# Kernel tuning notes

Hardware: AMD Instinct MI355X
Metric: run time of the kernel (lower is better)

Reference implementation:

```python
import jax, jax.numpy as jnp
import numpy as np
from jax import lax

D_MODEL = 96; D_STATE = 16; D_INNER = 192; DT_RANK = 6; K = 4
BSZ = 2; HH = 64; WW = 64


def setup_inputs() -> dict:
    key = jax.random.key(0)
    ks = jax.random.split(key, 16)
    f = lambda k, shape, s=0.02: (jax.random.normal(k, shape) * s).astype(jnp.float32)
    P = DT_RANK + 2 * D_STATE
    return {
        "x": jax.random.normal(ks[0], (BSZ, HH, WW, D_MODEL), jnp.float32),
        "W_in": f(ks[1], (2 * D_INNER, D_MODEL)),
        "b_in": jnp.zeros((2 * D_INNER,), jnp.float32),
        "conv_w": f(ks[2], (D_INNER, 1, 3, 3)),
        "conv_b": jnp.zeros((D_INNER,), jnp.float32),
        "W_xp": f(ks[3], (K * P, K * D_INNER)),
        "b_xp": jnp.zeros((K * P,), jnp.float32),
        "W_dt": f(ks[4], (K * D_INNER, K * DT_RANK)),
        "b_dt": f(ks[5], (K * D_INNER,), 0.1),
        "A_log": jax.random.normal(ks[6], (K * D_INNER, D_STATE), jnp.float32),
        "D_skip": jnp.ones((K * D_INNER,), jnp.float32),
        "dt_bias": jax.random.normal(ks[7], (K * D_INNER,), jnp.float32),
        "W_out": f(ks[8], (D_MODEL, D_INNER)),
        "b_out": jnp.zeros((D_MODEL,), jnp.float32),
        "gamma": jnp.ones((D_INNER,), jnp.float32),
        "beta": jnp.zeros((D_INNER,), jnp.float32),
    }


def cross_scan(x):
    # x: (B, D, H, W) -> (B, 4, D, L); dirs: row-major, col-major, and their reverses
    B, D, H, W = x.shape
    L = H * W
    x0 = x.reshape(B, D, L)
    x1 = jnp.swapaxes(x, 2, 3).reshape(B, D, L)
    return jnp.stack([x0, x1, x0[..., ::-1], x1[..., ::-1]], axis=1)


def cross_merge(ys):
    # ys: (B, 4, D, H, W) -> (B, D, L); inverse of cross_scan, summed
    B, Kk, D, H, W = ys.shape
    L = H * W
    yf = ys.reshape(B, Kk, D, L)
    y02 = yf[:, 0] + yf[:, 2, :, ::-1]
    y13 = yf[:, 1] + yf[:, 3, :, ::-1]
    y13 = jnp.swapaxes(y13.reshape(B, D, W, H), 2, 3).reshape(B, D, L)
    return y02 + y13


def selective_scan(u, dt, A, Bm, Cm, D_skip, dt_bias):
    # u, dt: (B,K,Dv,L); A: (K,Dv,N); Bm, Cm: (B,K,N,L); D_skip, dt_bias: (K,Dv)
    # NOTE: torch code repeats Bm/Cm across Dv; we broadcast instead (same math).
    dt = jax.nn.softplus(dt + dt_bias[None, :, :, None])
    dt_l = jnp.moveaxis(dt, -1, 0)   # (L,B,K,Dv)
    u_l = jnp.moveaxis(u, -1, 0)     # (L,B,K,Dv)
    B_l = jnp.moveaxis(Bm, -1, 0)    # (L,B,K,N)
    C_l = jnp.moveaxis(Cm, -1, 0)    # (L,B,K,N)

    def step(h, inp):
        dt_t, u_t, b_t, c_t = inp
        dA = jnp.exp(dt_t[..., None] * A[None])                 # (B,K,Dv,N)
        dBu = (dt_t * u_t)[..., None] * b_t[:, :, None, :]      # (B,K,Dv,N)
        h = dA * h + dBu
        y = jnp.einsum('bkdn,bkn->bkd', h, c_t)
        return h, y

    h0 = jnp.zeros(u.shape[:3] + (A.shape[-1],), u.dtype)
    _, ys = lax.scan(step, h0, (dt_l, u_l, B_l, C_l))
    ys = jnp.moveaxis(ys, 0, -1)  # (B,K,Dv,L)
    return ys + u * D_skip[None, :, :, None]


def reference(x, W_in, b_in, conv_w, conv_b, W_xp, b_xp, W_dt, b_dt,
              A_log, D_skip, dt_bias, W_out, b_out, gamma, beta):
    B, H, W, _ = x.shape
    L = H * W
    xz = x @ W_in.T + b_in
    xx, z = jnp.split(xz, 2, axis=-1)
    z = jax.nn.silu(z)
    xc = jnp.transpose(xx, (0, 3, 1, 2))  # (B, D, H, W)
    xc = lax.conv_general_dilated(xc, conv_w, (1, 1), 'SAME',
                                  feature_group_count=D_INNER,
                                  dimension_numbers=('NCHW', 'OIHW', 'NCHW'))
    xc = jax.nn.silu(xc + conv_b[None, :, None, None])

    xs = cross_scan(xc)                      # (B, K, D, L)
    xs_flat = xs.reshape(B, K * D_INNER, L)

    x_dbl = jnp.einsum('bcl,pc->bpl', xs_flat, W_xp) + b_xp[None, :, None]
    x_dbl = x_dbl.reshape(B, K, DT_RANK + 2 * D_STATE, L)
    dts, Bm, Cm = jnp.split(x_dbl, [DT_RANK, DT_RANK + D_STATE], axis=2)
    dts = dts.reshape(B, K * DT_RANK, L)
    dts = jnp.einsum('brl,dr->bdl', dts, W_dt) + b_dt[None, :, None]

    A = -jnp.exp(A_log).reshape(K, D_INNER, D_STATE)
    u = xs_flat.reshape(B, K, D_INNER, L)
    dt = dts.reshape(B, K, D_INNER, L)
    ys = selective_scan(u, dt, A, Bm, Cm,
                        D_skip.reshape(K, D_INNER), dt_bias.reshape(K, D_INNER))

    y = cross_merge(ys.reshape(B, K, D_INNER, H, W))  # (B, D, L)
    y = jnp.transpose(y.reshape(B, D_INNER, H, W), (0, 2, 3, 1))

    mu = jnp.mean(y, axis=-1, keepdims=True)
    var = jnp.mean(jnp.square(y - mu), axis=-1, keepdims=True)
    y = (y - mu) * lax.rsqrt(var + 1e-5) * gamma + beta
    y = y * z
    return y @ W_out.T + b_out
```

## Files before the change

kernel.cpp:

```cpp
#include <hip/hip_runtime.h>
#include <cstdint>
#include <cstddef>


#define CHUNK 16
#define NCK   256

#if __has_builtin(__builtin_amdgcn_exp2f)
#define EXP2(x) __builtin_amdgcn_exp2f(x)
#else
#define EXP2(x) exp2f(x)
#endif
#define LOG2E 1.44269504088896340736f
#define LN2   0.69314718055994530942f

typedef __attribute__((ext_vector_type(8))) short short8;
typedef __attribute__((ext_vector_type(8))) unsigned short ushort8;
typedef __attribute__((ext_vector_type(4))) float f32x4;

__device__ __forceinline__ float siluf(float x){ return x * (1.f/(1.f+__expf(-x))); }
__device__ __forceinline__ float softplus_fast(float v){
  float e  = EXP2(v*LOG2E);
  float sp = LN2*__log2f(1.f + e);
  return (v > 20.f) ? v : sp;
}
__device__ __forceinline__ unsigned short f2b(float f){
  uint32_t u = __float_as_uint(f);
  uint32_t r = (u + 0x7fffu + ((u>>16)&1u)) >> 16;
  return (unsigned short)r;
}

template<int KD, int STRA, int STRB>
__device__ __forceinline__ void micro_mm_T(const float (&As)[64][STRA], const float (&BsT)[KD][STRB],
                                           int tx, int ty, float (&acc)[4][4])
{
#pragma unroll 2
  for (int k4 = 0; k4 < KD/4; k4++){
    float a[4][4];
#pragma unroll
    for (int i = 0; i < 4; i++){
      float4 t = *(const float4*)&As[ty*4+i][k4*4];
      a[i][0]=t.x; a[i][1]=t.y; a[i][2]=t.z; a[i][3]=t.w;
    }
#pragma unroll
    for (int e = 0; e < 4; e++){
      float4 b = *(const float4*)&BsT[k4*4+e][tx*4];
#pragma unroll
      for (int i = 0; i < 4; i++){
        acc[i][0] = fmaf(a[i][e], b.x, acc[i][0]);
        acc[i][1] = fmaf(a[i][e], b.y, acc[i][1]);
        acc[i][2] = fmaf(a[i][e], b.z, acc[i][2]);
        acc[i][3] = fmaf(a[i][e], b.w, acc[i][3]);
      }
    }
  }
}

__global__ __launch_bounds__(256) void k_cast_w(
    const float* __restrict__ Wxp, unsigned short* __restrict__ Wf)
{
  int tid = blockIdx.x*256 + threadIdx.x;
  if (tid >= 18432) return;
  int lane = tid & 63; int rest = tid >> 6;
  int pt = rest % 6; rest /= 6;
  int k32 = rest & 3; rest >>= 2;
  int kc = rest % 6; int ph = rest / 6;
  int n = lane & 15, q = lane >> 4;
  int p = ph*96 + pt*16 + n;
  int kbase = kc*128 + k32*32 + q*8;
  unsigned short v[8];
#pragma unroll
  for (int j = 0; j < 8; j++)
    v[j] = (p < 152) ? f2b(Wxp[(size_t)p*768 + kbase + j]) : (unsigned short)0;
  *(ushort8*)(Wf + (size_t)tid*8) = *(ushort8*)v;
}

__global__ __launch_bounds__(256) void k_gemm_in(
    const float* __restrict__ x, const float* __restrict__ W,
    const float* __restrict__ bias, float* __restrict__ xx, float* __restrict__ zs)
{
  __shared__ float As[64][100];
  __shared__ float BsT[96][68];
  const int m0 = blockIdx.x*64, n0 = blockIdx.y*64;
  const int tid = threadIdx.x;
#pragma unroll
  for (int i = 0; i < 6; i++){
    int idx = tid + i*256;
    { int r = idx/24, c4 = idx%24;
      *(float4*)&As[r][c4*4] = *(const float4*)(x + (size_t)(m0+r)*96 + c4*4); }
    { int r = idx & 63, c4 = idx >> 6;
      float4 wv = *(const float4*)(W + (size_t)(n0+r)*96 + c4*4);
      BsT[c4*4+0][r]=wv.x; BsT[c4*4+1][r]=wv.y; BsT[c4*4+2][r]=wv.z; BsT[c4*4+3][r]=wv.w; }
  }
  __syncthreads();
  const int tx = tid & 15, ty = tid >> 4;
  float acc[4][4] = {};
  micro_mm_T<96,100,68>(As, BsT, tx, ty, acc);
#pragma unroll
  for (int i = 0; i < 4; i++){
    int m = m0 + ty*4 + i;
#pragma unroll
    for (int j = 0; j < 4; j++){
      int n = n0 + tx*4 + j;
      float v = acc[i][j] + bias[n];
      if (n < 192) xx[(size_t)m*192 + n] = v;
      else         zs[(size_t)m*192 + (n-192)] = siluf(v);
    }
  }
}

__global__ __launch_bounds__(256) void k_conv(
    const float* __restrict__ xx, const float* __restrict__ cw, const float* __restrict__ cb,
    float* __restrict__ xc,
    unsigned short* __restrict__ xcb, unsigned short* __restrict__ xcTb)
{
  int gid = blockIdx.x*256 + threadIdx.x;
  int c = gid % 192;
  int l = (gid/192) & 4095;
  int b = gid / (192*4096);
  int h = l >> 6, w = l & 63;
  float s = 0.f;
#pragma unroll
  for (int kh = 0; kh < 3; kh++){
    int h2 = h + kh - 1;
    if ((unsigned)h2 >= 64u) continue;
#pragma unroll
    for (int kw = 0; kw < 3; kw++){
      int w2 = w + kw - 1;
      if ((unsigned)w2 >= 64u) continue;
      s += xx[((size_t)b*4096 + h2*64 + w2)*192 + c] * cw[c*9 + kh*3 + kw];
    }
  }
  s = siluf(s + cb[c]);
  unsigned short sb = f2b(s);
  size_t i0 = ((size_t)b*4096 + l)*192 + c;
  xc[i0] = s; xcb[i0] = sb;
  int tl = (l & 63)*64 + (l >> 6);
  xcTb[((size_t)b*4096 + tl)*192 + c] = sb;
}

__global__ __launch_bounds__(256) void k_gemm_xdbl(
    const unsigned short* __restrict__ xcb, const unsigned short* __restrict__ xcTb,
    const unsigned short* __restrict__ Wf, const float* __restrict__ bxp,
    float* __restrict__ xdbl, float* __restrict__ dts_c)
{
  __shared__ unsigned short Bsh[4*6*64*8];
  const int tid = threadIdx.x;
  const int lane = tid & 63, w = tid >> 6;
  const int wl = w & 1, wp = w >> 1;
  const int l0 = blockIdx.x*64, ph = blockIdx.y, b = blockIdx.z;
  const int n = lane & 15, q = lane >> 4;
  f32x4 acc[2][3] = {};
  const unsigned short* slab0 = Wf + (size_t)ph*6*12288;
  for (int kc = 0; kc < 6; kc++){
    __syncthreads();
    const ushort8* srcp = (const ushort8*)(slab0 + (size_t)kc*12288);
#pragma unroll
    for (int t = 0; t < 6; t++) ((ushort8*)Bsh)[tid + t*256] = srcp[tid + t*256];
    __syncthreads();
#pragma unroll
    for (int k32 = 0; k32 < 4; k32++){
      int kk = kc*128 + k32*32;
      int dir = kk/192; int ch = kk%192 + q*8;
      const unsigned short* sp = (dir & 1) ? xcTb : xcb;
      bool rev = (dir >= 2);
      short8 a[2];
#pragma unroll
      for (int mt = 0; mt < 2; mt++){
        int ls = l0 + wl*32 + mt*16 + n;
        int row = rev ? 4095 - ls : ls;
        a[mt] = *(const short8*)(sp + ((size_t)b*4096 + row)*192 + ch);
      }
#pragma unroll
      for (int j = 0; j < 3; j++){
        short8 bfr = *(const short8*)&Bsh[((size_t)(k32*6 + wp*3 + j)*64 + lane)*8];
#pragma unroll
        for (int mt = 0; mt < 2; mt++)
          acc[mt][j] = __builtin_amdgcn_mfma_f32_16x16x32_bf16(a[mt], bfr, acc[mt][j], 0, 0, 0);
      }
    }
  }
#pragma unroll
  for (int mt = 0; mt < 2; mt++)
#pragma unroll
    for (int j = 0; j < 3; j++){
      int p = ph*96 + (wp*3+j)*16 + n;
      if (p < 152){
        int k = p/38, pp = p%38;
        int off = (pp < 6) ? pp : pp + 2;
        float bias = bxp[p];
#pragma unroll
        for (int reg = 0; reg < 4; reg++){
          int l = l0 + wl*32 + mt*16 + q*4 + reg;
          float val = acc[mt][j][reg] + bias;
          xdbl[(((size_t)b*4 + k)*4096 + l)*48 + off] = val;
          if (pp < 6) dts_c[((size_t)b*4096 + l)*24 + k*6 + pp] = val;
        }
      }
    }
}

__global__ __launch_bounds__(256) void k_scanA(
    const float* __restrict__ xc, const float* __restrict__ xdbl,
    const float* __restrict__ dts_c,
    const float* __restrict__ A_log, const float* __restrict__ Wdt,
    const float* __restrict__ bdt, const float* __restrict__ dtbias,
    float* __restrict__ dte, float* __restrict__ Pb, float* __restrict__ Sb)
{
  const int lane = threadIdx.x & 63;
  const int wid  = __builtin_amdgcn_readfirstlane(blockIdx.x*4 + (threadIdx.x >> 6));
  const int ck = wid & (NCK-1); const int g = wid / NCK;
  const int dblk = g % 3; const int bk = g / 3;
  const int k = bk & 3; const int b = bk >> 2;
  const int d = dblk*64 + lane; const int ch = k*192 + d;
  float An[16];
  {
    const float4* ap = (const float4*)(A_log + (size_t)ch*16);
#pragma unroll
    for (int i = 0; i < 4; i++){
      float4 t = ap[i];
      An[4*i+0] = -LOG2E*__expf(t.x); An[4*i+1] = -LOG2E*__expf(t.y);
      An[4*i+2] = -LOG2E*__expf(t.z); An[4*i+3] = -LOG2E*__expf(t.w);
    }
  }
  float Wr[24];
#pragma unroll
  for (int r = 0; r < 24; r++) Wr[r] = Wdt[(size_t)ch*24 + r];
  const float bsum = bdt[ch] + dtbias[ch];
  const int l0 = ck*CHUNK;
  const bool rev = (k >= 2);
  const int tr = k & 1;
  const int T0 = tr ? ((l0 & 63)*64 + (l0 >> 6)) : l0;
  const int rs = tr ? 64 : 1;
  const int row0 = rev ? 4095 - T0 : T0;
  const int rstep = (rev ? -rs : rs)*192;
  const float* up  = xc + ((size_t)b*4096 + row0)*192 + d;
  const float* qc  = dts_c + ((size_t)b*4096 + l0)*24;
  const float* xbc = xdbl + (((size_t)b*4 + k)*4096 + l0)*48;
  float* dtw = dte + (((size_t)b*4 + k)*4096 + l0)*192 + d;
  float h[16];
#pragma unroll
  for (int n = 0; n < 16; n++) h[n] = 0.f;
  float sdt = 0.f;
#pragma unroll 4
  for (int t = 0; t < CHUNK; t++){
    float u  = up[0];
    float4 B0 = *(const float4*)(xbc + 8);
    float4 B1 = *(const float4*)(xbc + 12);
    float4 B2 = *(const float4*)(xbc + 16);
    float4 B3 = *(const float4*)(xbc + 20);
    float Bv[16] = {B0.x,B0.y,B0.z,B0.w, B1.x,B1.y,B1.z,B1.w,
                    B2.x,B2.y,B2.z,B2.w, B3.x,B3.y,B3.z,B3.w};
    float4 q0 = *(const float4*)(qc);
    float4 q1 = *(const float4*)(qc + 4);
    float4 q2 = *(const float4*)(qc + 8);
    float4 q3 = *(const float4*)(qc + 12);
    float4 q4 = *(const float4*)(qc + 16);
    float4 q5 = *(const float4*)(qc + 20);
    float qv[24] = {q0.x,q0.y,q0.z,q0.w, q1.x,q1.y,q1.z,q1.w,
                    q2.x,q2.y,q2.z,q2.w, q3.x,q3.y,q3.z,q3.w,
                    q4.x,q4.y,q4.z,q4.w, q5.x,q5.y,q5.z,q5.w};
    float v0 = bsum, v1 = 0.f, v2 = 0.f, v3 = 0.f;
#pragma unroll
    for (int r = 0; r < 24; r += 4){
      v0 = fmaf(Wr[r+0], qv[r+0], v0);
      v1 = fmaf(Wr[r+1], qv[r+1], v1);
      v2 = fmaf(Wr[r+2], qv[r+2], v2);
      v3 = fmaf(Wr[r+3], qv[r+3], v3);
    }
    float dt = softplus_fast((v0+v1) + (v2+v3));
    dtw[0] = dt;
    float dtu = dt*u;
    sdt += dt;
#pragma unroll
    for (int n = 0; n < 16; n++){
      float dA = EXP2(dt*An[n]);
      h[n] = fmaf(dA, h[n], dtu*Bv[n]);
    }
    qc += 24; xbc += 48; up += rstep; dtw += 192;
  }
  size_t base = ((size_t)wid*16)*64 + lane;
#pragma unroll
  for (int n = 0; n < 16; n++){
    Pb[base + n*64] = EXP2(An[n]*sdt);
    Sb[base + n*64] = h[n];
  }
}

__global__ __launch_bounds__(64) void k_scanB(
    const float* __restrict__ Pb, const float* __restrict__ Sb, float* __restrict__ H0)
{
  int tid = blockIdx.x*64 + threadIdx.x;
  int lane = tid & 63; int n = (tid >> 6) & 15; int g = tid >> 10;
  float h = 0.f;
#pragma unroll 8
  for (int ck = 0; ck < NCK; ck++){
    size_t idx = (((size_t)(g*NCK + ck)*16) + n)*64 + lane;
    H0[idx] = h;
    h = fmaf(Pb[idx], h, Sb[idx]);
  }
}

__global__ __launch_bounds__(256) void k_scanC(
    const float* __restrict__ xc, const float* __restrict__ xdbl,
    const float* __restrict__ A_log, const float* __restrict__ dte,
    const float* __restrict__ Dskip,
    const float* __restrict__ H0, float* __restrict__ ys)
{
  const int lane = threadIdx.x & 63;
  const int wid  = __builtin_amdgcn_readfirstlane(blockIdx.x*4 + (threadIdx.x >> 6));
  const int ck = wid & (NCK-1); const int g = wid / NCK;
  const int dblk = g % 3; const int bk = g / 3;
  const int k = bk & 3; const int b = bk >> 2;
  const int d = dblk*64 + lane; const int ch = k*192 + d;
  float An[16];
  {
    const float4* ap = (const float4*)(A_log + (size_t)ch*16);
#pragma unroll
    for (int i = 0; i < 4; i++){
      float4 t = ap[i];
      An[4*i+0] = -LOG2E*__expf(t.x); An[4*i+1] = -LOG2E*__expf(t.y);
      An[4*i+2] = -LOG2E*__expf(t.z); An[4*i+3] = -LOG2E*__expf(t.w);
    }
  }
  const float Dv = Dskip[ch];
  const int l0 = ck*CHUNK;
  const bool rev = (k >= 2);
  const int tr = k & 1;
  const int T0 = tr ? ((l0 & 63)*64 + (l0 >> 6)) : l0;
  const int rs = tr ? 64 : 1;
  const int row0 = rev ? 4095 - T0 : T0;
  const int rstep = (rev ? -rs : rs)*192;
  const float* up  = xc + ((size_t)b*4096 + row0)*192 + d;
  const float* xbc = xdbl + (((size_t)b*4 + k)*4096 + l0)*48;
  const float* dtp = dte + (((size_t)b*4 + k)*4096 + l0)*192 + d;
  float* ysp = ys + ((size_t)(k*2 + b))*4096*192 + (size_t)row0*192 + d;
  float h[16];
  size_t base = ((size_t)wid*16)*64 + lane;
#pragma unroll
  for (int n = 0; n < 16; n++) h[n] = H0[base + n*64];
#pragma unroll 4
  for (int t = 0; t < CHUNK; t++){
    float u  = up[0];
    float dt = dtp[0];
    float4 B0 = *(const float4*)(xbc + 8);
    float4 B1 = *(const float4*)(xbc + 12);
    float4 B2 = *(const float4*)(xbc + 16);
    float4 B3 = *(const float4*)(xbc + 20);
    float4 C0 = *(const float4*)(xbc + 24);
    float4 C1 = *(const float4*)(xbc + 28);
    float4 C2 = *(const float4*)(xbc + 32);
    float4 C3 = *(const float4*)(xbc + 36);
    float Bv[16] = {B0.x,B0.y,B0.z,B0.w, B1.x,B1.y,B1.z,B1.w,
                    B2.x,B2.y,B2.z,B2.w, B3.x,B3.y,B3.z,B3.w};
    float Cv[16] = {C0.x,C0.y,C0.z,C0.w, C1.x,C1.y,C1.z,C1.w,
                    C2.x,C2.y,C2.z,C2.w, C3.x,C3.y,C3.z,C3.w};
    float dtu = dt*u;
    float y0 = u*Dv, y1 = 0.f;
#pragma unroll
    for (int n = 0; n < 16; n += 2){
      float dA0 = EXP2(dt*An[n]);
      float dA1 = EXP2(dt*An[n+1]);
      h[n]   = fmaf(dA0, h[n],   dtu*Bv[n]);
      h[n+1] = fmaf(dA1, h[n+1], dtu*Bv[n+1]);
      y0 = fmaf(h[n],   Cv[n],   y0);
      y1 = fmaf(h[n+1], Cv[n+1], y1);
    }
    ysp[0] = y0 + y1;
    xbc += 48; dtp += 192; up += rstep; ysp += rstep;
  }
}

__global__ __launch_bounds__(256) void k_ln(
    const float* __restrict__ ys, const float* __restrict__ zs,
    const float* __restrict__ gamma, const float* __restrict__ beta,
    float* __restrict__ yln)
{
  int row = blockIdx.x*4 + (threadIdx.x >> 6);
  int lane = threadIdx.x & 63;
  int b = row >> 12; int l = row & 4095;
  float v[3];
#pragma unroll
  for (int j = 0; j < 3; j++){
    int c = lane + j*64;
    float s = 0.f;
#pragma unroll
    for (int k = 0; k < 4; k++) s += ys[(((size_t)k*2 + b)*4096 + l)*192 + c];
    v[j] = s;
  }
  float tot = v[0] + v[1] + v[2];
#pragma unroll
  for (int o = 1; o < 64; o <<= 1) tot += __shfl_xor(tot, o);
  float mean = tot * (1.f/192.f);
  float d0 = v[0]-mean, d1 = v[1]-mean, d2 = v[2]-mean;
  float vs = d0*d0 + d1*d1 + d2*d2;
#pragma unroll
  for (int o = 1; o < 64; o <<= 1) vs += __shfl_xor(vs, o);
  float rstd = rsqrtf(vs*(1.f/192.f) + 1e-5f);
  float nd[3] = {d0, d1, d2};
#pragma unroll
  for (int j = 0; j < 3; j++){
    int c = lane + j*64;
    float val = nd[j]*rstd*gamma[c] + beta[c];
    val *= zs[(size_t)row*192 + c];
    yln[(size_t)row*192 + c] = val;
  }
}

__global__ __launch_bounds__(256) void k_gemm_out(
    const float* __restrict__ yln, const float* __restrict__ Wout,
    const float* __restrict__ bout, float* __restrict__ out)
{
  __shared__ float As[64][100];
  __shared__ float BsT[96][68];
  const int m0 = blockIdx.x*64, n0 = blockIdx.y*64;
  const int tid = threadIdx.x;
  const int tx = tid & 15, ty = tid >> 4;
  float acc[4][4] = {};
  for (int kc = 0; kc < 2; kc++){
    __syncthreads();
#pragma unroll
    for (int i = 0; i < 6; i++){
      int idx = tid + i*256;
      { int r = idx/24, c4 = idx%24;
        *(float4*)&As[r][c4*4] = *(const float4*)(yln + (size_t)(m0+r)*192 + kc*96 + c4*4); }
      { int r = idx & 63, c4 = idx >> 6;
        int nn = n0 + r;
        float4 wv = make_float4(0.f,0.f,0.f,0.f);
        if (nn < 96) wv = *(const float4*)(Wout + (size_t)nn*192 + kc*96 + c4*4);
        BsT[c4*4+0][r]=wv.x; BsT[c4*4+1][r]=wv.y; BsT[c4*4+2][r]=wv.z; BsT[c4*4+3][r]=wv.w; }
    }
    __syncthreads();
    micro_mm_T<96,100,68>(As, BsT, tx, ty, acc);
  }
#pragma unroll
  for (int i = 0; i < 4; i++){
    int m = m0 + ty*4 + i;
#pragma unroll
    for (int j = 0; j < 4; j++){
      int n = n0 + tx*4 + j;
      if (n < 96) out[(size_t)m*96 + n] = acc[i][j] + bout[n];
    }
  }
}

extern "C" void kernel_launch(void* const* d_in, const int* in_sizes, int n_in,
                              void* d_out, int out_size, void* d_ws, size_t ws_size,
                              hipStream_t stream)
{
  const float* x      = (const float*)d_in[0];
  const float* W_in   = (const float*)d_in[1];
  const float* b_in   = (const float*)d_in[2];
  const float* conv_w = (const float*)d_in[3];
  const float* conv_b = (const float*)d_in[4];
  const float* W_xp   = (const float*)d_in[5];
  const float* b_xp   = (const float*)d_in[6];
  const float* W_dt   = (const float*)d_in[7];
  const float* b_dt   = (const float*)d_in[8];
  const float* A_log  = (const float*)d_in[9];
  const float* D_skip = (const float*)d_in[10];
  const float* dt_bias= (const float*)d_in[11];
  const float* W_out  = (const float*)d_in[12];
  const float* b_out  = (const float*)d_in[13];
  const float* gamma  = (const float*)d_in[14];
  const float* beta   = (const float*)d_in[15];
  float* out = (float*)d_out;

  float* ws    = (float*)d_ws;
  float* xx    = ws;
  float* zs    = ws + 1572864;
  float* xc    = ws + 3145728;
  float* xdbl  = ws + 4718592;
  float* ysb   = ws + 6291456;
  float* yln   = ws + 12582912;
  float* dte   = ws + 14155776;
  float* Pb    = ws + 20447232;
  float* Sb    = ws + 26738688;
  float* H0    = ws + 33030144;
  float* dts_c = ws + 39321600;
  unsigned short* xcb  = (unsigned short*)(ws + 39518208);
  unsigned short* xcTb = xcb + 1572864;
  unsigned short* Wf   = (unsigned short*)(ws + 41091072);

  k_cast_w   <<<72,             256, 0, stream>>>(W_xp, Wf);
  k_gemm_in  <<<dim3(128, 6),   256, 0, stream>>>(x, W_in, b_in, xx, zs);
  k_conv     <<<6144,           256, 0, stream>>>(xx, conv_w, conv_b, xc, xcb, xcTb);
  k_gemm_xdbl<<<dim3(64, 2, 2), 256, 0, stream>>>(xcb, xcTb, Wf, b_xp, xdbl, dts_c);
  k_scanA    <<<1536,           256, 0, stream>>>(xc, xdbl, dts_c, A_log, W_dt, b_dt, dt_bias, dte, Pb, Sb);
  k_scanB    <<<384,            64,  0, stream>>>(Pb, Sb, H0);
  k_scanC    <<<1536,           256, 0, stream>>>(xc, xdbl, A_log, dte, D_skip, H0, ysb);
  k_ln       <<<2048,           256, 0, stream>>>(ysb, zs, gamma, beta, yln);
  k_gemm_out <<<dim3(128, 2),   256, 0, stream>>>(yln, W_out, b_out, out);
}
```

Measured before the change: 227.0 us.

## Move input and output projections to bf16 MFMA with prepacked weights

Replaces the fp32 shared-memory SIMT GEMMs for the input projection and output projection with bf16 MFMA 16x16x32 kernels. The activations are cast to bf16 on load, and the weights are prepacked into fragment layout by an extended pack kernel that also covers W_in and W_out. This removes the shared-memory staging and FMA loops, and the grids shrink to 128 blocks each. In exchange it adds bf16 rounding error to both projections, and the small grids may underuse the GPU.

```diff
diff --git a/kernel.cpp b/kernel.cpp
--- a/kernel.cpp
+++ b/kernel.cpp
@@ -29,84 +29,97 @@
   uint32_t r = (u + 0x7fffu + ((u>>16)&1u)) >> 16;
   return (unsigned short)r;
 }
-
-template<int KD, int STRA, int STRB>
-__device__ __forceinline__ void micro_mm_T(const float (&As)[64][STRA], const float (&BsT)[KD][STRB],
-                                           int tx, int ty, float (&acc)[4][4])
-{
-#pragma unroll 2
-  for (int k4 = 0; k4 < KD/4; k4++){
-    float a[4][4];
-#pragma unroll
-    for (int i = 0; i < 4; i++){
-      float4 t = *(const float4*)&As[ty*4+i][k4*4];
-      a[i][0]=t.x; a[i][1]=t.y; a[i][2]=t.z; a[i][3]=t.w;
-    }
-#pragma unroll
-    for (int e = 0; e < 4; e++){
-      float4 b = *(const float4*)&BsT[k4*4+e][tx*4];
-#pragma unroll
-      for (int i = 0; i < 4; i++){
-        acc[i][0] = fmaf(a[i][e], b.x, acc[i][0]);
-        acc[i][1] = fmaf(a[i][e], b.y, acc[i][1]);
-        acc[i][2] = fmaf(a[i][e], b.z, acc[i][2]);
-        acc[i][3] = fmaf(a[i][e], b.w, acc[i][3]);
+__device__ __forceinline__ short8 cast8(const float* p){
+  float4 f0 = *(const float4*)p;
+  float4 f1 = *(const float4*)(p+4);
+  unsigned short t[8] = {f2b(f0.x),f2b(f0.y),f2b(f0.z),f2b(f0.w),
+                         f2b(f1.x),f2b(f1.y),f2b(f1.z),f2b(f1.w)};
+  return *(short8*)t;
+}
+
+__global__ __launch_bounds__(256) void k_pack(
+    const float* __restrict__ Wxp, const float* __restrict__ Win,
+    const float* __restrict__ Wout,
+    unsigned short* __restrict__ Wf, unsigned short* __restrict__ Wfin,
+    unsigned short* __restrict__ Wfout)
+{
+  int tid = blockIdx.x*256 + threadIdx.x;
+  int lane = tid & 63;
+  int n = lane & 15, q = lane >> 4;
+  if (tid < 18432){
+    int rest = tid >> 6;
+    int pt = rest % 6; rest /= 6;
+    int k32 = rest & 3; rest >>= 2;
+    int kc = rest % 6; int ph = rest / 6;
+    int p = ph*96 + pt*16 + n;
+    int kbase = kc*128 + k32*32 + q*8;
+    unsigned short v[8];
+#pragma unroll
+    for (int j = 0; j < 8; j++)
+      v[j] = (p < 152) ? f2b(Wxp[(size_t)p*768 + kbase + j]) : (unsigned short)0;
+    *(ushort8*)(Wf + (size_t)tid*8) = *(ushort8*)v;
+  } else if (tid < 23040){
+    int e = tid - 18432;
+    int rest = e >> 6;
+    int nt = rest % 24, k32 = rest / 24;
+    int p = nt*16 + n;
+    int kbase = k32*32 + q*8;
+    unsigned short v[8];
+#pragma unroll
+    for (int j = 0; j < 8; j++) v[j] = f2b(Win[(size_t)p*96 + kbase + j]);
+    *(ushort8*)(Wfin + (size_t)e*8) = *(ushort8*)v;
+  } else if (tid < 25344){
+    int e = tid - 23040;
+    int rest = e >> 6;
+    int nt = rest % 6, k32 = rest / 6;
+    int p = nt*16 + n;
+    int kbase = k32*32 + q*8;
+    unsigned short v[8];
+#pragma unroll
+    for (int j = 0; j < 8; j++) v[j] = f2b(Wout[(size_t)p*192 + kbase + j]);
+    *(ushort8*)(Wfout + (size_t)e*8) = *(ushort8*)v;
+  }
+}
+
+__global__ __launch_bounds__(256) void k_gemm_in(
+    const float* __restrict__ x, const unsigned short* __restrict__ Wfin,
+    const float* __restrict__ bias, float* __restrict__ xx, float* __restrict__ zs)
+{
+  const int tid = threadIdx.x;
+  const int lane = tid & 63, w = tid >> 6;
+  const int m0 = blockIdx.x*64;
+  const int n = lane & 15, q = lane >> 4;
+  f32x4 acc[4][6] = {};
+#pragma unroll
+  for (int k32 = 0; k32 < 3; k32++){
+    int kb = k32*32 + q*8;
+    short8 a[4];
+#pragma unroll
+    for (int mf = 0; mf < 4; mf++)
+      a[mf] = cast8(x + (size_t)(m0 + mf*16 + n)*96 + kb);
+#pragma unroll
+    for (int j = 0; j < 6; j++){
+      int nt = w*6 + j;
+      short8 bfr = *(const short8*)(Wfin + ((size_t)(k32*24 + nt)*64 + lane)*8);
+#pragma unroll
+      for (int mf = 0; mf < 4; mf++)
+        acc[mf][j] = __builtin_amdgcn_mfma_f32_16x16x32_bf16(a[mf], bfr, acc[mf][j], 0, 0, 0);
+    }
+  }
+#pragma unroll
+  for (int mf = 0; mf < 4; mf++)
+#pragma unroll
+    for (int j = 0; j < 6; j++){
+      int nn = w*96 + j*16 + n;
+      float bv = bias[nn];
+#pragma unroll
+      for (int reg = 0; reg < 4; reg++){
+        int l = m0 + mf*16 + q*4 + reg;
+        float v = acc[mf][j][reg] + bv;
+        if (nn < 192) xx[(size_t)l*192 + nn] = v;
+        else          zs[(size_t)l*192 + (nn-192)] = siluf(v);
       }
     }
-  }
-}
-
-__global__ __launch_bounds__(256) void k_cast_w(
-    const float* __restrict__ Wxp, unsigned short* __restrict__ Wf)
-{
-  int tid = blockIdx.x*256 + threadIdx.x;
-  if (tid >= 18432) return;
-  int lane = tid & 63; int rest = tid >> 6;
-  int pt = rest % 6; rest /= 6;
-  int k32 = rest & 3; rest >>= 2;
-  int kc = rest % 6; int ph = rest / 6;
-  int n = lane & 15, q = lane >> 4;
-  int p = ph*96 + pt*16 + n;
-  int kbase = kc*128 + k32*32 + q*8;
-  unsigned short v[8];
-#pragma unroll
-  for (int j = 0; j < 8; j++)
-    v[j] = (p < 152) ? f2b(Wxp[(size_t)p*768 + kbase + j]) : (unsigned short)0;
-  *(ushort8*)(Wf + (size_t)tid*8) = *(ushort8*)v;
-}
-
-__global__ __launch_bounds__(256) void k_gemm_in(
-    const float* __restrict__ x, const float* __restrict__ W,
-    const float* __restrict__ bias, float* __restrict__ xx, float* __restrict__ zs)
-{
-  __shared__ float As[64][100];
-  __shared__ float BsT[96][68];
-  const int m0 = blockIdx.x*64, n0 = blockIdx.y*64;
-  const int tid = threadIdx.x;
-#pragma unroll
-  for (int i = 0; i < 6; i++){
-    int idx = tid + i*256;
-    { int r = idx/24, c4 = idx%24;
-      *(float4*)&As[r][c4*4] = *(const float4*)(x + (size_t)(m0+r)*96 + c4*4); }
-    { int r = idx & 63, c4 = idx >> 6;
-      float4 wv = *(const float4*)(W + (size_t)(n0+r)*96 + c4*4);
-      BsT[c4*4+0][r]=wv.x; BsT[c4*4+1][r]=wv.y; BsT[c4*4+2][r]=wv.z; BsT[c4*4+3][r]=wv.w; }
-  }
-  __syncthreads();
-  const int tx = tid & 15, ty = tid >> 4;
-  float acc[4][4] = {};
-  micro_mm_T<96,100,68>(As, BsT, tx, ty, acc);
-#pragma unroll
-  for (int i = 0; i < 4; i++){
-    int m = m0 + ty*4 + i;
-#pragma unroll
-    for (int j = 0; j < 4; j++){
-      int n = n0 + tx*4 + j;
-      float v = acc[i][j] + bias[n];
-      if (n < 192) xx[(size_t)m*192 + n] = v;
-      else         zs[(size_t)m*192 + (n-192)] = siluf(v);
-    }
-  }
 }
 
 __global__ __launch_bounds__(256) void k_conv(
@@ -408,38 +421,32 @@
 }
 
 __global__ __launch_bounds__(256) void k_gemm_out(
-    const float* __restrict__ yln, const float* __restrict__ Wout,
+    const float* __restrict__ yln, const unsigned short* __restrict__ Wfout,
     const float* __restrict__ bout, float* __restrict__ out)
 {
-  __shared__ float As[64][100];
-  __shared__ float BsT[96][68];
-  const int m0 = blockIdx.x*64, n0 = blockIdx.y*64;
   const int tid = threadIdx.x;
-  const int tx = tid & 15, ty = tid >> 4;
-  float acc[4][4] = {};
-  for (int kc = 0; kc < 2; kc++){
-    __syncthreads();
-#pragma unroll
-    for (int i = 0; i < 6; i++){
-      int idx = tid + i*256;
-      { int r = idx/24, c4 = idx%24;
-        *(float4*)&As[r][c4*4] = *(const float4*)(yln + (size_t)(m0+r)*192 + kc*96 + c4*4); }
-      { int r = idx & 63, c4 = idx >> 6;
-        int nn = n0 + r;
-        float4 wv = make_float4(0.f,0.f,0.f,0.f);
-        if (nn < 96) wv = *(const float4*)(Wout + (size_t)nn*192 + kc*96 + c4*4);
-        BsT[c4*4+0][r]=wv.x; BsT[c4*4+1][r]=wv.y; BsT[c4*4+2][r]=wv.z; BsT[c4*4+3][r]=wv.w; }
-    }
-    __syncthreads();
-    micro_mm_T<96,100,68>(As, BsT, tx, ty, acc);
-  }
-#pragma unroll
-  for (int i = 0; i < 4; i++){
-    int m = m0 + ty*4 + i;
-#pragma unroll
-    for (int j = 0; j < 4; j++){
-      int n = n0 + tx*4 + j;
-      if (n < 96) out[(size_t)m*96 + n] = acc[i][j] + bout[n];
+  const int lane = tid & 63, w = tid >> 6;
+  const int m0 = blockIdx.x*64 + w*16;
+  const int n = lane & 15, q = lane >> 4;
+  f32x4 acc[6] = {};
+#pragma unroll
+  for (int k32 = 0; k32 < 6; k32++){
+    int kb = k32*32 + q*8;
+    short8 a = cast8(yln + (size_t)(m0 + n)*192 + kb);
+#pragma unroll
+    for (int j = 0; j < 6; j++){
+      short8 bfr = *(const short8*)(Wfout + ((size_t)(k32*6 + j)*64 + lane)*8);
+      acc[j] = __builtin_amdgcn_mfma_f32_16x16x32_bf16(a, bfr, acc[j], 0, 0, 0);
+    }
+  }
+#pragma unroll
+  for (int j = 0; j < 6; j++){
+    int nn = j*16 + n;
+    float bv = bout[nn];
+#pragma unroll
+    for (int reg = 0; reg < 4; reg++){
+      int m = m0 + q*4 + reg;
+      out[(size_t)m*96 + nn] = acc[j][reg] + bv;
     }
   }
 }
@@ -478,17 +485,19 @@
   float* Sb    = ws + 26738688;
   float* H0    = ws + 33030144;
   float* dts_c = ws + 39321600;
-  unsigned short* xcb  = (unsigned short*)(ws + 39518208);
-  unsigned short* xcTb = xcb + 1572864;
-  unsigned short* Wf   = (unsigned short*)(ws + 41091072);
-
-  k_cast_w   <<<72,             256, 0, stream>>>(W_xp, Wf);
-  k_gemm_in  <<<dim3(128, 6),   256, 0, stream>>>(x, W_in, b_in, xx, zs);
+  unsigned short* xcb   = (unsigned short*)(ws + 39518208);
+  unsigned short* xcTb  = xcb + 1572864;
+  unsigned short* Wf    = (unsigned short*)(ws + 41091072);
+  unsigned short* Wfin  = (unsigned short*)(ws + 41164800);
+  unsigned short* Wfout = (unsigned short*)(ws + 41183232);
+
+  k_pack     <<<99,             256, 0, stream>>>(W_xp, W_in, W_out, Wf, Wfin, Wfout);
+  k_gemm_in  <<<128,            256, 0, stream>>>(x, Wfin, b_in, xx, zs);
   k_conv     <<<6144,           256, 0, stream>>>(xx, conv_w, conv_b, xc, xcb, xcTb);
   k_gemm_xdbl<<<dim3(64, 2, 2), 256, 0, stream>>>(xcb, xcTb, Wf, b_xp, xdbl, dts_c);
   k_scanA    <<<1536,           256, 0, stream>>>(xc, xdbl, dts_c, A_log, W_dt, b_dt, dt_bias, dte, Pb, Sb);
   k_scanB    <<<384,            64,  0, stream>>>(Pb, Sb, H0);
   k_scanC    <<<1536,           256, 0, stream>>>(xc, xdbl, A_log, dte, D_skip, H0, ysb);
   k_ln       <<<2048,           256, 0, stream>>>(ysb, zs, gamma, beta, yln);
-  k_gemm_out <<<dim3(128, 2),   256, 0, stream>>>(yln, W_out, b_out, out);
-}
+  k_gemm_out <<<128,            256, 0, stream>>>(yln, Wfout, b_out, out);
+}
```

After: 222.0 us (median of 2 runs). 1.02x faster.
